# Performance work log

Measured on AMD Instinct MI355X. Metric: run time of the kernel, lower is better.

Reference implementation:

```python
import jax, jax.numpy as jnp
import numpy as np

B, Q, K, D, H = 8, 128, 1024, 256, 256


def setup_inputs() -> dict:
    key = jax.random.key(0)
    ks = jax.random.split(key, 7)
    queries = jax.random.normal(ks[0], (B, Q, D), dtype=jnp.float32)
    keys = jax.random.normal(ks[1], (B, K, D), dtype=jnp.float32)
    values = jax.random.normal(ks[2], (B, K, D), dtype=jnp.float32)
    W_q = jax.random.normal(ks[3], (H, D), dtype=jnp.float32) * (1.0 / np.sqrt(D))
    W_k = jax.random.normal(ks[4], (H, D), dtype=jnp.float32) * (1.0 / np.sqrt(D))
    w_v = jax.random.normal(ks[5], (H,), dtype=jnp.float32) * (1.0 / np.sqrt(H))
    valid_lens = jax.random.randint(ks[6], (B,), 0, K, dtype=jnp.int64)
    return {"queries": queries, "keys": keys, "values": values,
            "W_q": W_q, "W_k": W_k, "w_v": w_v, "valid_lens": valid_lens}


def reference(queries, keys, values, W_q, W_k, w_v, valid_lens):
    # Linear projections (bias=False): [B,Q,H], [B,K,H]
    q = jnp.einsum("bqd,hd->bqh", queries, W_q)
    k = jnp.einsum("bkd,hd->bkh", keys, W_k)
    # Broadcast add -> tanh -> reduce with w_v: scores [B,Q,K]
    features = jnp.tanh(q[:, :, None, :] + k[:, None, :, :])  # [B,Q,K,H]
    scores = jnp.einsum("bqkh,h->bqk", features, w_v)
    # Masked softmax over K: positions >= valid_len get -1e9
    mask = jnp.arange(K)[None, None, :] < valid_lens[:, None, None]
    scores = jnp.where(mask, scores, jnp.float32(-1e9))
    attn = jax.nn.softmax(scores, axis=-1)  # [B,Q,K]
    # Dropout p=0.0 (eval): identity. bmm(attn, values) -> [B,Q,Dv]
    return jnp.einsum("bqk,bkv->bqv", attn, values)
```

## Files before the change

### kernel.cpp

```cpp
#include <hip/hip_runtime.h>

#define BB 8
#define QQ 128
#define KK 1024
#define DD 256
#define HH 256

#define KSP 32
#define KCH 32

#define ZSP 4
#define RTOT (BB * QQ + BB * KK)
#define PSTRIDE ((size_t)RTOT * HH)

#define TWO_LOG2E     2.8853900817779268f
#define NEG_TWO_LOG2E -2.8853900817779268f

__global__ __launch_bounds__(256) void proj_kernel(const float* __restrict__ queries,
                                                   const float* __restrict__ keys,
                                                   const float* __restrict__ Wq,
                                                   const float* __restrict__ Wk,
                                                   const int* __restrict__ vlen,
                                                   float* __restrict__ pp) {
    const int r0 = blockIdx.x * 64;
    const bool isQ = (r0 < BB * QQ);
    if (!isQ) {
        const int kb = (r0 - BB * QQ) >> 6;
        const int b  = kb >> 4;
        const int k0 = (kb & 15) << 6;
        if (k0 >= vlen[b]) return;
    }

    __shared__ float smem[192 * 68];
    float (*As)[68] = (float(*)[68])smem;
    float (*Ws)[68] = (float(*)[68])(smem + 64 * 68);

    const int t  = threadIdx.x;
    const int tr = t & 15;
    const int th = t >> 4;
    const int h0 = blockIdx.y * 128;
    const int dc = blockIdx.z * 64;
    const float* A = isQ ? (queries + (size_t)r0 * DD)
                         : (keys + (size_t)(r0 - BB * QQ) * DD);
    const float* W = isQ ? Wq : Wk;

#pragma unroll
    for (int i = 0; i < 4; ++i) {
        int fi  = t + 256 * i;
        int row = fi >> 4;
        int c4  = (fi & 15) << 2;
        *(float4*)&As[row][c4] = *(const float4*)&A[(size_t)row * DD + dc + c4];
    }
#pragma unroll
    for (int i = 0; i < 8; ++i) {
        int fi  = t + 256 * i;
        int row = fi >> 4;
        int c4  = (fi & 15) << 2;
        *(float4*)&Ws[row][c4] = *(const float4*)&W[(size_t)(h0 + row) * DD + dc + c4];
    }
    __syncthreads();

    float acc[4][8] = {};
#pragma unroll 2
    for (int dd = 0; dd < 64; dd += 4) {
        float4 a4[4], w4[8];
#pragma unroll
        for (int i = 0; i < 4; ++i) a4[i] = *(float4*)&As[tr + 16 * i][dd];
#pragma unroll
        for (int j = 0; j < 8; ++j) w4[j] = *(float4*)&Ws[th + 16 * j][dd];
#pragma unroll
        for (int i = 0; i < 4; ++i)
#pragma unroll
            for (int j = 0; j < 8; ++j) {
                acc[i][j] += a4[i].x * w4[j].x + a4[i].y * w4[j].y +
                             a4[i].z * w4[j].z + a4[i].w * w4[j].w;
            }
    }
    __syncthreads();

    float (*Ob)[132] = (float(*)[132])smem;
#pragma unroll
    for (int i = 0; i < 4; ++i)
#pragma unroll
        for (int j = 0; j < 8; ++j)
            Ob[tr + 16 * i][th + 16 * j] = TWO_LOG2E * acc[i][j];
    __syncthreads();

    float* outp = pp + (size_t)blockIdx.z * PSTRIDE + (size_t)r0 * HH + h0;
#pragma unroll
    for (int i = 0; i < 8; ++i) {
        int fi  = t + 256 * i;
        int row = fi >> 5;
        int c4  = (fi & 31) << 2;
        *(float4*)&outp[(size_t)row * HH + c4] = *(float4*)&Ob[row][c4];
    }
}

__global__ __launch_bounds__(512, 4) void scoreav_kernel(const float* __restrict__ pp,
                                                         const float* __restrict__ wv,
                                                         const int* __restrict__ vlen,
                                                         const float* __restrict__ V,
                                                         float* __restrict__ partial,
                                                         float* __restrict__ psum) {
    int id = blockIdx.x;
    int b = 0;
    bool found = false;
#pragma unroll
    for (int bb = 0; bb < BB; ++bb) {
        if (!found) {
            int v = vlen[bb];
            int cnt = ((v == 0) ? KSP : ((v + KCH - 1) / KCH)) * 4;
            if (id < cnt) { b = bb; found = true; }
            else id -= cnt;
        }
    }
    if (!found) return;
    const int ksb = id >> 2;
    const int q0  = (id & 3) * 32;
    const int k0  = ksb * KCH;
    const int vl  = vlen[b];

    __shared__ float st[2][32][260];
    __shared__ float pT[KCH][36];
    float* red = &st[0][0][0];

    const int t = threadIdx.x;
    const int w = t >> 6;
    const int l = t & 63;
    const int ql = l & 7;
    const int kl = l >> 3;

    float acc[4][4] = {};

    if (vl > 0) {
#pragma unroll
        for (int i = 0; i < 8; ++i) {
            int fi  = t + 512 * i;
            int row = fi >> 6;
            int c4  = (fi & 63) << 2;
            size_t gr = (row < 32) ? (size_t)(b * QQ + q0 + row)
                                   : (size_t)(BB * QQ + b * KK + k0 + row - 32);
            const float* base = pp + gr * HH + c4;
            float4 v0 = *(const float4*)base;
            float4 v1 = *(const float4*)(base + PSTRIDE);
            float4 v2 = *(const float4*)(base + 2 * PSTRIDE);
            float4 v3 = *(const float4*)(base + 3 * PSTRIDE);
            float4 s;
            s.x = __builtin_amdgcn_exp2f((v0.x + v1.x) + (v2.x + v3.x));
            s.y = __builtin_amdgcn_exp2f((v0.y + v1.y) + (v2.y + v3.y));
            s.z = __builtin_amdgcn_exp2f((v0.z + v1.z) + (v2.z + v3.z));
            s.w = __builtin_amdgcn_exp2f((v0.w + v1.w) + (v2.w + v3.w));
            *(float4*)&st[row >> 5][row & 31][c4] = s;
        }
        __syncthreads();

        const int hw = 32 * w;
#pragma unroll
        for (int hh = 0; hh < 32; hh += 4) {
            const float4 w4 = *(const float4*)&wv[hw + hh];
            const float* wa = (const float*)&w4;
            float4 q4[4], k4[4];
#pragma unroll
            for (int i = 0; i < 4; ++i) q4[i] = *(float4*)&st[0][ql + 8 * i][hw + hh];
#pragma unroll
            for (int j = 0; j < 4; ++j) k4[j] = *(float4*)&st[1][kl + 8 * j][hw + hh];
#pragma unroll
            for (int i = 0; i < 4; ++i) {
                const float* qa = (const float*)&q4[i];
#pragma unroll
                for (int j = 0; j < 4; ++j) {
                    const float* ka = (const float*)&k4[j];
#pragma unroll
                    for (int c = 0; c < 4; ++c) {
                        float d = __builtin_fmaf(qa[c], ka[c], 1.0f);
                        acc[i][j] += wa[c] * __builtin_amdgcn_rcpf(d);
                    }
                }
            }
        }
        __syncthreads();

#pragma unroll
        for (int i = 0; i < 4; ++i)
#pragma unroll
            for (int j = 0; j < 4; ++j)
                red[w * 1056 + (ql + 8 * i) * 33 + (kl + 8 * j)] = acc[i][j];
    }
    __syncthreads();

    float pvv[2];
#pragma unroll
    for (int u = 0; u < 2; ++u) {
        int n = t + 512 * u;
        int q = n >> 5, k = n & 31;
        float s = 0.f;
        if (vl > 0) {
#pragma unroll
            for (int ww = 0; ww < 8; ++ww) s += red[ww * 1056 + q * 33 + k];
        }
        int kg = k0 + k;
        float pv;
        if (vl == 0) pv = 1.0f;
        else pv = (kg < vl) ? __builtin_amdgcn_exp2f(NEG_TWO_LOG2E * s) : 0.0f;
        pT[k][q] = pv;
        pvv[u] = pv;
    }
    float s0 = pvv[0], s1 = pvv[1];
#pragma unroll
    for (int off = 1; off < 32; off <<= 1) {
        s0 += __shfl_xor(s0, off);
        s1 += __shfl_xor(s1, off);
    }
    if ((l & 31) == 0) {
        int qa = 2 * w + (l >> 5);
        psum[((size_t)ksb * BB + b) * QQ + q0 + qa]      = s0;
        psum[((size_t)ksb * BB + b) * QQ + q0 + qa + 16] = s1;
    }
    __syncthreads();

    const float* VB = V + ((size_t)b * KK + k0) * DD;
    const int d4 = (t & 63) << 2;
    const int qg = w << 2;
    float4 a4[4] = {};
#pragma unroll 4
    for (int k = 0; k < KCH; ++k) {
        float4 v4 = *(const float4*)&VB[(size_t)k * DD + d4];
        float4 p4 = *(float4*)&pT[k][qg];
        a4[0].x += p4.x * v4.x; a4[0].y += p4.x * v4.y; a4[0].z += p4.x * v4.z; a4[0].w += p4.x * v4.w;
        a4[1].x += p4.y * v4.x; a4[1].y += p4.y * v4.y; a4[1].z += p4.y * v4.z; a4[1].w += p4.y * v4.w;
        a4[2].x += p4.z * v4.x; a4[2].y += p4.z * v4.y; a4[2].z += p4.z * v4.z; a4[2].w += p4.z * v4.w;
        a4[3].x += p4.w * v4.x; a4[3].y += p4.w * v4.y; a4[3].z += p4.w * v4.z; a4[3].w += p4.w * v4.w;
    }
#pragma unroll
    for (int qi = 0; qi < 4; ++qi) {
        int q = q0 + qg + qi;
        *(float4*)&partial[(((size_t)ksb * BB + b) * QQ + q) * DD + d4] = a4[qi];
    }
}

__global__ __launch_bounds__(256) void av_reduce(const float* __restrict__ partial,
                                                 const float* __restrict__ psum,
                                                 const int* __restrict__ vlen,
                                                 float* __restrict__ out) {
    const int i  = blockIdx.x * 256 + threadIdx.x;
    const int bq = i >> 6;
    const int b  = bq >> 7;
    const int vl = vlen[b];
    const int nch = (vl == 0) ? KSP : ((vl + KCH - 1) / KCH);

    const float4* p4 = (const float4*)partial;
    const int stride4 = BB * QQ * DD / 4;

    float S = 0.f;
    float4 s = {0.f, 0.f, 0.f, 0.f};
    int ks = 0;
    for (; ks + 4 <= nch; ks += 4) {
        float Sa = psum[(size_t)(ks + 0) * (BB * QQ) + bq];
        float Sb = psum[(size_t)(ks + 1) * (BB * QQ) + bq];
        float Sc = psum[(size_t)(ks + 2) * (BB * QQ) + bq];
        float Sd = psum[(size_t)(ks + 3) * (BB * QQ) + bq];
        float4 x0 = p4[(size_t)(ks + 0) * stride4 + i];
        float4 x1 = p4[(size_t)(ks + 1) * stride4 + i];
        float4 x2 = p4[(size_t)(ks + 2) * stride4 + i];
        float4 x3 = p4[(size_t)(ks + 3) * stride4 + i];
        S += (Sa + Sb) + (Sc + Sd);
        s.x += (x0.x + x1.x) + (x2.x + x3.x);
        s.y += (x0.y + x1.y) + (x2.y + x3.y);
        s.z += (x0.z + x1.z) + (x2.z + x3.z);
        s.w += (x0.w + x1.w) + (x2.w + x3.w);
    }
    for (; ks < nch; ++ks) {
        S += psum[(size_t)ks * (BB * QQ) + bq];
        float4 x = p4[(size_t)ks * stride4 + i];
        s.x += x.x; s.y += x.y; s.z += x.z; s.w += x.w;
    }

    const float inv = 1.0f / S;
    s.x *= inv; s.y *= inv; s.z *= inv; s.w *= inv;
    ((float4*)out)[i] = s;
}

extern "C" void kernel_launch(void* const* d_in, const int* in_sizes, int n_in,
                              void* d_out, int out_size, void* d_ws, size_t ws_size,
                              hipStream_t stream) {
    const float* queries = (const float*)d_in[0];
    const float* keys    = (const float*)d_in[1];
    const float* values  = (const float*)d_in[2];
    const float* W_q     = (const float*)d_in[3];
    const float* W_k     = (const float*)d_in[4];
    const float* w_v     = (const float*)d_in[5];
    const int*   vlen    = (const int*)d_in[6];
    float* out = (float*)d_out;

    float* ws      = (float*)d_ws;
    float* pp      = ws;
    float* psum    = pp + (size_t)ZSP * PSTRIDE;
    float* partial = psum + (size_t)KSP * BB * QQ;

    proj_kernel<<<dim3(RTOT / 64, HH / 128, ZSP), 256, 0, stream>>>(
        queries, keys, W_q, W_k, vlen, pp);

    scoreav_kernel<<<dim3(KSP * 4 * BB, 1, 1), 512, 0, stream>>>(
        pp, w_v, vlen, values, partial, psum);

    av_reduce<<<dim3(BB * QQ * DD / 4 / 256, 1, 1), 256, 0, stream>>>(
        partial, psum, vlen, out);
}
```

Baseline: 129.6 us.

## Precompute combined exp projections in a separate kernel and double-buffer proj LDS reads

Adds a combine_kernel that sums the four split-K projection partials and applies exp2 once per row, writing a single buffer. scoreav_kernel then loads that buffer directly instead of re-reading four partials and recomputing exp for every tile. Before this, each query row was recomputed across many K tiles and each key row across the four Q tiles. The cost is an extra launch plus a round trip through global memory for the combined buffer. Separately, the projection GEMM inner loop is fully unrolled with register double-buffering of the shared-memory operand reads, which raises register pressure.

```diff
diff --git a/kernel.cpp b/kernel.cpp
--- a/kernel.cpp
+++ b/kernel.cpp
@@ -61,19 +61,28 @@
     __syncthreads();
 
     float acc[4][8] = {};
-#pragma unroll 2
+    float4 a4[2][4], w4[2][8];
+#pragma unroll
+    for (int i = 0; i < 4; ++i) a4[0][i] = *(float4*)&As[tr + 16 * i][0];
+#pragma unroll
+    for (int j = 0; j < 8; ++j) w4[0][j] = *(float4*)&Ws[th + 16 * j][0];
+
+#pragma unroll
     for (int dd = 0; dd < 64; dd += 4) {
-        float4 a4[4], w4[8];
-#pragma unroll
-        for (int i = 0; i < 4; ++i) a4[i] = *(float4*)&As[tr + 16 * i][dd];
-#pragma unroll
-        for (int j = 0; j < 8; ++j) w4[j] = *(float4*)&Ws[th + 16 * j][dd];
+        const int cur = (dd >> 2) & 1;
+        const int nxt = cur ^ 1;
+        if (dd + 4 < 64) {
+#pragma unroll
+            for (int i = 0; i < 4; ++i) a4[nxt][i] = *(float4*)&As[tr + 16 * i][dd + 4];
+#pragma unroll
+            for (int j = 0; j < 8; ++j) w4[nxt][j] = *(float4*)&Ws[th + 16 * j][dd + 4];
+        }
 #pragma unroll
         for (int i = 0; i < 4; ++i)
 #pragma unroll
             for (int j = 0; j < 8; ++j) {
-                acc[i][j] += a4[i].x * w4[j].x + a4[i].y * w4[j].y +
-                             a4[i].z * w4[j].z + a4[i].w * w4[j].w;
+                acc[i][j] += a4[cur][i].x * w4[cur][j].x + a4[cur][i].y * w4[cur][j].y +
+                             a4[cur][i].z * w4[cur][j].z + a4[cur][i].w * w4[cur][j].w;
             }
     }
     __syncthreads();
@@ -96,7 +105,31 @@
     }
 }
 
-__global__ __launch_bounds__(512, 4) void scoreav_kernel(const float* __restrict__ pp,
+__global__ __launch_bounds__(256) void combine_kernel(const float* __restrict__ pp,
+                                                      const int* __restrict__ vlen,
+                                                      float* __restrict__ ppc) {
+    const int row = blockIdx.x * 4 + (threadIdx.x >> 6);
+    const int l   = threadIdx.x & 63;
+    if (row >= BB * QQ) {
+        const int rk = row - BB * QQ;
+        const int b  = rk >> 10;
+        const int k  = rk & (KK - 1);
+        if (k >= vlen[b]) return;
+    }
+    const float* base = pp + (size_t)row * HH + (l << 2);
+    float4 v0 = *(const float4*)base;
+    float4 v1 = *(const float4*)(base + PSTRIDE);
+    float4 v2 = *(const float4*)(base + 2 * PSTRIDE);
+    float4 v3 = *(const float4*)(base + 3 * PSTRIDE);
+    float4 s;
+    s.x = __builtin_amdgcn_exp2f((v0.x + v1.x) + (v2.x + v3.x));
+    s.y = __builtin_amdgcn_exp2f((v0.y + v1.y) + (v2.y + v3.y));
+    s.z = __builtin_amdgcn_exp2f((v0.z + v1.z) + (v2.z + v3.z));
+    s.w = __builtin_amdgcn_exp2f((v0.w + v1.w) + (v2.w + v3.w));
+    *(float4*)&ppc[(size_t)row * HH + (l << 2)] = s;
+}
+
+__global__ __launch_bounds__(512, 4) void scoreav_kernel(const float* __restrict__ ppc,
                                                          const float* __restrict__ wv,
                                                          const int* __restrict__ vlen,
                                                          const float* __restrict__ V,
@@ -140,17 +173,8 @@
             int c4  = (fi & 63) << 2;
             size_t gr = (row < 32) ? (size_t)(b * QQ + q0 + row)
                                    : (size_t)(BB * QQ + b * KK + k0 + row - 32);
-            const float* base = pp + gr * HH + c4;
-            float4 v0 = *(const float4*)base;
-            float4 v1 = *(const float4*)(base + PSTRIDE);
-            float4 v2 = *(const float4*)(base + 2 * PSTRIDE);
-            float4 v3 = *(const float4*)(base + 3 * PSTRIDE);
-            float4 s;
-            s.x = __builtin_amdgcn_exp2f((v0.x + v1.x) + (v2.x + v3.x));
-            s.y = __builtin_amdgcn_exp2f((v0.y + v1.y) + (v2.y + v3.y));
-            s.z = __builtin_amdgcn_exp2f((v0.z + v1.z) + (v2.z + v3.z));
-            s.w = __builtin_amdgcn_exp2f((v0.w + v1.w) + (v2.w + v3.w));
-            *(float4*)&st[row >> 5][row & 31][c4] = s;
+            *(float4*)&st[row >> 5][row & 31][c4] =
+                *(const float4*)&ppc[gr * HH + c4];
         }
         __syncthreads();
 
@@ -294,14 +318,17 @@
 
     float* ws      = (float*)d_ws;
     float* pp      = ws;
-    float* psum    = pp + (size_t)ZSP * PSTRIDE;
+    float* ppc     = pp + (size_t)ZSP * PSTRIDE;
+    float* psum    = ppc + PSTRIDE;
     float* partial = psum + (size_t)KSP * BB * QQ;
 
     proj_kernel<<<dim3(RTOT / 64, HH / 128, ZSP), 256, 0, stream>>>(
         queries, keys, W_q, W_k, vlen, pp);
 
+    combine_kernel<<<dim3(RTOT / 4, 1, 1), 256, 0, stream>>>(pp, vlen, ppc);
+
     scoreav_kernel<<<dim3(KSP * 4 * BB, 1, 1), 512, 0, stream>>>(
-        pp, w_v, vlen, values, partial, psum);
+        ppc, w_v, vlen, values, partial, psum);
 
     av_reduce<<<dim3(BB * QQ * DD / 4 / 256, 1, 1), 256, 0, stream>>>(
         partial, psum, vlen, out);
```

Result: no change. 131.0 us (+1.0%).
